# Optimization experiments

Hardware: AMD Instinct MI355X
Metric: run time of the kernel (lower is better)

## Reference

```python
import jax, jax.numpy as jnp
import numpy as np

EMBED_DIM = 256
NUM_EMB = 4096
LIMIT = 0.01


def setup_inputs() -> dict:
    key = jax.random.key(0)
    k1, k2 = jax.random.split(key)
    x = jax.random.normal(k1, (32, 32, 32, EMBED_DIM), dtype=jnp.float32)
    # codebook initialized uniform(-limit, limit), stored as [D, K] like the torch module
    vectors = jax.random.uniform(k2, (EMBED_DIM, NUM_EMB), dtype=jnp.float32,
                                 minval=-LIMIT, maxval=LIMIT)
    return {"x": x, "vectors": vectors}


def reference(x, vectors):
    B = x.shape[0]
    flat_x = x.reshape(-1, EMBED_DIM)                       # [N, D]
    distances = (jnp.sum(flat_x * flat_x, axis=1, keepdims=True)
                 - 2.0 * flat_x @ vectors
                 + jnp.sum(vectors * vectors, axis=0, keepdims=True))
    encoding_indices = jnp.argmin(distances, axis=1)        # [N]
    quantized_flat = vectors.T[encoding_indices]            # gather rows of [K, D]
    quantized_x = quantized_flat.reshape(x.shape)
    dictionary_loss = jnp.mean((jax.lax.stop_gradient(x) - quantized_x) ** 2)
    commitment_loss = jnp.mean((x - jax.lax.stop_gradient(quantized_x)) ** 2)
    # straight-through estimator
    quantized_x = x + jax.lax.stop_gradient(quantized_x - x)
    return (quantized_x, dictionary_loss, commitment_loss,
            encoding_indices.reshape(B, -1))
```

## Files before the change

kernel.cpp:

```cpp
#include <hip/hip_runtime.h>
#include <math.h>

#define D_DIM 256
#define K_NUM 4096
#define N_ROWS 32768
#define QCAP 3072
#define MARGIN 0.02f

typedef _Float16 half8 __attribute__((ext_vector_type(8)));
typedef float floatx4 __attribute__((ext_vector_type(4)));

__global__ __launch_bounds__(256) void vq_vv(const float* __restrict__ V,
                                             float* __restrict__ vv) {
  int k = blockIdx.x * 256 + threadIdx.x;
  float acc = 0.0f;
  for (int d = 0; d < D_DIM; ++d) {
    float v = V[(size_t)d * K_NUM + k];
    acc = __fadd_rn(acc, __fmul_rn(v, v));
  }
  vv[k] = acc;
}

__global__ __launch_bounds__(256) void vq_prep(const float* __restrict__ V,
                                               _Float16* __restrict__ vtb,
                                               float* __restrict__ vt,
                                               int write_vt) {
  __shared__ float tile[64][64];
  const int col0 = (blockIdx.x & 63) * 64;
  const int d0 = (blockIdx.x >> 6) * 64;
  const int cq = threadIdx.x >> 6;
  const int cl = threadIdx.x & 63;
#pragma unroll
  for (int it = 0; it < 16; ++it) {
    int d = it * 4 + cq;
    tile[d][cl] = V[(size_t)(d0 + d) * K_NUM + col0 + cl];
  }
  __syncthreads();
#pragma unroll
  for (int qq = 0; qq < 2; ++qq) {
    int q = cq * 2 + qq;
    half8 h;
#pragma unroll
    for (int j = 0; j < 8; ++j) h[j] = (_Float16)tile[q * 8 + j][cl];
    *(half8*)(vtb + ((size_t)(d0 / 8 + q) * K_NUM + col0 + cl) * 8) = h;
  }
  if (write_vt) {
#pragma unroll
    for (int j = 0; j < 4; ++j) {
      int d = cq * 16 + j * 4;
      float4 f;
      f.x = tile[d + 0][cl]; f.y = tile[d + 1][cl];
      f.z = tile[d + 2][cl]; f.w = tile[d + 3][cl];
      *(float4*)(vt + (size_t)(col0 + cl) * D_DIM + d0 + d) = f;
    }
  }
}

struct alignas(16) ScreenShared {
  _Float16 a[64 * 256];
  float vvs[K_NUM];
  float xxs[64];
  float wmin[8][64];
  float thr[64];
  unsigned long long best[64];
  unsigned qbuf[QCAP];
  int qn;
};

__device__ __forceinline__ void vq_push(ScreenShared& sh, int r, int col) {
  int u = atomicAdd(&sh.qn, 1);
  if (u < QCAP) sh.qbuf[u] = ((unsigned)r << 12) | (unsigned)col;
}

template <int MODE>
__device__ __forceinline__ void vq_cell(ScreenShared& sh,
                                        const _Float16* __restrict__ vtb,
                                        float* tb, int w, int l, int c) {
  const int g = l >> 4, ln = l & 15;
  const int cb = w * 512 + c * 32;
  const float vv0 = sh.vvs[cb + ln];
  const float vv1 = sh.vvs[cb + 16 + ln];

  const int abase = (ln << 8) ^ ((g ^ (ln & 7)) << 3);
  const char* bp = (const char*)vtb + (((size_t)g * K_NUM + cb + ln) << 4);

  floatx4 acc[4][2];
#pragma unroll
  for (int rf = 0; rf < 4; ++rf)
#pragma unroll
    for (int cf = 0; cf < 2; ++cf) acc[rf][cf] = {0.f, 0.f, 0.f, 0.f};

  half8 afb[2][4], bfb[2][2];
  bfb[0][0] = *(const half8*)bp;
  bfb[0][1] = *(const half8*)(bp + 256);
#pragma unroll
  for (int rf = 0; rf < 4; ++rf)
    afb[0][rf] = *(const half8*)(sh.a + abase + rf * 4096);

#pragma unroll
  for (int ks = 0; ks < 8; ++ks) {
    const int cur = ks & 1, nxt = cur ^ 1;
    if (ks < 7) {
      const int koff = (ks + 1) * 262144;
      bfb[nxt][0] = *(const half8*)(bp + koff);
      bfb[nxt][1] = *(const half8*)(bp + koff + 256);
      const int aoff = abase ^ ((ks + 1) << 5);
#pragma unroll
      for (int rf = 0; rf < 4; ++rf)
        afb[nxt][rf] = *(const half8*)(sh.a + aoff + rf * 4096);
    }
#pragma unroll
    for (int rf = 0; rf < 4; ++rf)
#pragma unroll
      for (int cf = 0; cf < 2; ++cf)
        acc[rf][cf] = __builtin_amdgcn_mfma_f32_16x16x32_f16(
            afb[cur][rf], bfb[cur][cf], acc[rf][cf], 0, 0, 0);
  }

#pragma unroll
  for (int rf = 0; rf < 4; ++rf) {
#pragma unroll
    for (int reg = 0; reg < 4; ++reg) {
      float s0v = fmaf(-2.0f, acc[rf][0][reg], vv0);
      float s1v = fmaf(-2.0f, acc[rf][1][reg], vv1);
      float m = fminf(s0v, s1v);
      if (MODE == 0) {
        tb[rf * 4 + reg] = fminf(tb[rf * 4 + reg], m);
      } else {
        float thr = tb[rf * 4 + reg];
        if (m <= thr) {
          const int r = rf * 16 + g * 4 + reg;
          if (s0v <= thr) vq_push(sh, r, cb + ln);
          if (s1v <= thr) vq_push(sh, r, cb + 16 + ln);
        }
      }
    }
  }
}

__global__ __launch_bounds__(512, 4) void vq_screen(
    const float* __restrict__ X, const float* __restrict__ V,
    const _Float16* __restrict__ vtb, const float* __restrict__ vvp,
    const float* __restrict__ vt, float* __restrict__ idx_out,
    float* __restrict__ outq, float* __restrict__ loss_sum) {
  __shared__ ScreenShared sh;
  const int tid = threadIdx.x;
  const int w = tid >> 6, l = tid & 63;
  const int row0 = blockIdx.x * 64;

#pragma unroll
  for (int it = 0; it < 4; ++it) {
    int idx = it * 512 + tid;
    int r = idx >> 5, s = idx & 31;
    const float* xp = X + (size_t)(row0 + r) * D_DIM + s * 8;
    float4 v0 = *(const float4*)xp, v1 = *(const float4*)(xp + 4);
    half8 h;
    h[0] = (_Float16)v0.x; h[1] = (_Float16)v0.y;
    h[2] = (_Float16)v0.z; h[3] = (_Float16)v0.w;
    h[4] = (_Float16)v1.x; h[5] = (_Float16)v1.y;
    h[6] = (_Float16)v1.z; h[7] = (_Float16)v1.w;
    int slot = (r << 5) | (s ^ (r & 7));
    *(half8*)&sh.a[slot * 8] = h;
  }
#pragma unroll
  for (int it = 0; it < 8; ++it) sh.vvs[it * 512 + tid] = vvp[it * 512 + tid];

  {
    const int grp = tid >> 4;
    const int half = (l >> 3) & 1, j = l & 7;
#pragma unroll
    for (int rr = 0; rr < 2; ++rr) {
      const int r = grp * 2 + rr;
      const float* p = X + (size_t)(row0 + r) * D_DIM + half * 128 + j;
      float v = p[0];
      float acc = __fmul_rn(v, v);
#pragma unroll
      for (int i = 1; i < 16; ++i) {
        v = p[i * 8];
        acc = __fadd_rn(acc, __fmul_rn(v, v));
      }
      acc = __fadd_rn(acc, __shfl_xor(acc, 1));
      acc = __fadd_rn(acc, __shfl_xor(acc, 2));
      acc = __fadd_rn(acc, __shfl_xor(acc, 4));
      acc = __fadd_rn(acc, __shfl_xor(acc, 8));
      if ((l & 15) == 0) sh.xxs[r] = acc;
    }
  }
  if (tid < 64) sh.best[tid] = 0xFFFFFFFFFFFFFFFFull;
  if (tid == 0) sh.qn = 0;
  __syncthreads();

  float tb[16];
#pragma unroll
  for (int i = 0; i < 16; ++i) tb[i] = INFINITY;

  vq_cell<0>(sh, vtb, tb, w, l, 0);
  vq_cell<0>(sh, vtb, tb, w, l, 8);

#pragma unroll
  for (int i = 0; i < 16; ++i) {
#pragma unroll
    for (int off = 1; off <= 8; off <<= 1)
      tb[i] = fminf(tb[i], __shfl_xor(tb[i], off));
  }
  {
    const int g = l >> 4, ln = l & 15;
    if (ln == 0) {
#pragma unroll
      for (int rf = 0; rf < 4; ++rf)
#pragma unroll
        for (int reg = 0; reg < 4; ++reg)
          sh.wmin[w][rf * 16 + g * 4 + reg] = tb[rf * 4 + reg];
    }
  }
  __syncthreads();
  if (tid < 64) {
    float m = sh.wmin[0][tid];
#pragma unroll
    for (int j = 1; j < 8; ++j) m = fminf(m, sh.wmin[j][tid]);
    sh.thr[tid] = m + MARGIN;
  }
  __syncthreads();
  {
    const int g = l >> 4;
#pragma unroll
    for (int rf = 0; rf < 4; ++rf)
#pragma unroll
      for (int reg = 0; reg < 4; ++reg)
        tb[rf * 4 + reg] = sh.thr[rf * 16 + g * 4 + reg];
  }

  for (int c = 0; c < 16; ++c) vq_cell<1>(sh, vtb, tb, w, l, c);
  __syncthreads();

  const int nq = min(sh.qn, QCAP);
  for (int i = w; i < nq; i += 8) {
    unsigned e = sh.qbuf[i];
    int r = (int)(e >> 12), col = (int)(e & 4095);
    float4 xv = *(const float4*)(X + (size_t)(row0 + r) * D_DIM + l * 4);
    float p = 0.f;
    if (vt) {
      float4 qv = *(const float4*)(vt + (size_t)col * D_DIM + l * 4);
      p = fmaf(xv.x, qv.x, p);
      p = fmaf(xv.y, qv.y, p);
      p = fmaf(xv.z, qv.z, p);
      p = fmaf(xv.w, qv.w, p);
    } else {
      const float* vp = V + col;
      p = fmaf(xv.x, vp[(size_t)(l * 4 + 0) * K_NUM], p);
      p = fmaf(xv.y, vp[(size_t)(l * 4 + 1) * K_NUM], p);
      p = fmaf(xv.z, vp[(size_t)(l * 4 + 2) * K_NUM], p);
      p = fmaf(xv.w, vp[(size_t)(l * 4 + 3) * K_NUM], p);
    }
#pragma unroll
    for (int off = 1; off < 64; off <<= 1) p += __shfl_xor(p, off);
    if (l == 0) {
      float s = __fadd_rn(__fsub_rn(sh.xxs[r], __fmul_rn(2.0f, p)),
                          sh.vvs[col]);
      unsigned long long key =
          ((unsigned long long)__float_as_uint(s) << 32) | (unsigned)col;
      atomicMin(&sh.best[r], key);
    }
  }
  __syncthreads();

  if (tid < 64)
    idx_out[row0 + tid] = (float)(unsigned)(sh.best[tid] & 0xFFFFFFFFu);

  float lsum = 0.f;
#pragma unroll
  for (int it = 0; it < 8; ++it) {
    int t = it * 512 + tid;
    int rloc = t >> 6;
    int c4 = (t & 63) << 2;
    int bi = (int)(unsigned)(sh.best[rloc] & 0xFFFFFFFFu);
    float4 xv = *(const float4*)(X + (size_t)(row0 + rloc) * D_DIM + c4);
    float4 qv;
    if (vt) {
      qv = *(const float4*)(vt + (size_t)bi * D_DIM + c4);
    } else {
      qv.x = V[(size_t)(c4 + 0) * K_NUM + bi];
      qv.y = V[(size_t)(c4 + 1) * K_NUM + bi];
      qv.z = V[(size_t)(c4 + 2) * K_NUM + bi];
      qv.w = V[(size_t)(c4 + 3) * K_NUM + bi];
    }
    float4 o;
    o.x = __fadd_rn(xv.x, __fsub_rn(qv.x, xv.x));
    o.y = __fadd_rn(xv.y, __fsub_rn(qv.y, xv.y));
    o.z = __fadd_rn(xv.z, __fsub_rn(qv.z, xv.z));
    o.w = __fadd_rn(xv.w, __fsub_rn(qv.w, xv.w));
    *(float4*)(outq + (size_t)(row0 + rloc) * D_DIM + c4) = o;
    float d0 = __fsub_rn(xv.x, qv.x), d1 = __fsub_rn(xv.y, qv.y);
    float d2 = __fsub_rn(xv.z, qv.z), d3 = __fsub_rn(xv.w, qv.w);
    lsum += d0 * d0 + d1 * d1 + d2 * d2 + d3 * d3;
  }
#pragma unroll
  for (int off = 1; off < 64; off <<= 1) lsum += __shfl_xor(lsum, off);
  __syncthreads();
  float* red = (float*)sh.qbuf;
  if (l == 0) red[w] = lsum;
  __syncthreads();
  if (tid == 0) {
    float s = red[0];
#pragma unroll
    for (int j = 1; j < 8; ++j) s += red[j];
    atomicAdd(loss_sum, s);
  }
}

__global__ void vq_fin(const float* __restrict__ loss_sum,
                       float* __restrict__ out_losses) {
  float m = loss_sum[0] / 8388608.0f;
  out_losses[0] = m;
  out_losses[1] = m;
}

extern "C" void kernel_launch(void* const* d_in, const int* in_sizes, int n_in,
                              void* d_out, int out_size, void* d_ws, size_t ws_size,
                              hipStream_t stream) {
  const float* x = (const float*)d_in[0];
  const float* V = (const float*)d_in[1];
  float* out = (float*)d_out;
  float* outq    = out;
  float* outloss = out + 8388608;
  float* outidx  = out + 8388610;

  float* ws_vv  = (float*)d_ws;
  float* ws_sum = ws_vv + K_NUM;
  _Float16* ws_vtb = (_Float16*)((char*)d_ws + 163840);
  float* ws_vt = (float*)((char*)d_ws + 163840 + 2097152);
  const int have_vt = (ws_size >= (size_t)(163840 + 2097152 + 4194304));
  float* vt_arg = have_vt ? ws_vt : (float*)nullptr;

  hipMemsetAsync(ws_sum, 0, sizeof(float), stream);
  vq_vv    <<<K_NUM / 256, 256, 0, stream>>>(V, ws_vv);
  vq_prep  <<<256, 256, 0, stream>>>(V, ws_vtb, ws_vt, have_vt);
  vq_screen<<<N_ROWS / 64, 512, 0, stream>>>(x, V, ws_vtb, ws_vv, vt_arg,
                                             outidx, outq, ws_sum);
  vq_fin   <<<1, 1, 0, stream>>>(ws_sum, outloss);
}
```

Measured before the change: 196.7 us.

## Triple-buffer codebook fragments, raise MFMA priority, use nontemporal epilogue memory ops

The B-fragment prefetch in the MFMA distance cell moves from double to triple buffering, so global codebook loads are issued two k-steps ahead. The MFMA block is wrapped in s_setprio to favour matrix issue over other waves. The rescoring and output epilogue now use nontemporal loads and stores for X, the transposed codebook, and the quantized output, to reduce cache pollution. Together these add register pressure and may lower occupancy. The nontemporal hint on the reused codebook rows could also hurt cache hits.

```diff
diff --git a/kernel.cpp b/kernel.cpp
--- a/kernel.cpp
+++ b/kernel.cpp
@@ -90,31 +90,36 @@
 #pragma unroll
     for (int cf = 0; cf < 2; ++cf) acc[rf][cf] = {0.f, 0.f, 0.f, 0.f};
 
-  half8 afb[2][4], bfb[2][2];
+  half8 afb[2][4], bfb[3][2];
   bfb[0][0] = *(const half8*)bp;
   bfb[0][1] = *(const half8*)(bp + 256);
+  bfb[1][0] = *(const half8*)(bp + 262144);
+  bfb[1][1] = *(const half8*)(bp + 262144 + 256);
 #pragma unroll
   for (int rf = 0; rf < 4; ++rf)
     afb[0][rf] = *(const half8*)(sh.a + abase + rf * 4096);
 
 #pragma unroll
   for (int ks = 0; ks < 8; ++ks) {
-    const int cur = ks & 1, nxt = cur ^ 1;
+    if (ks < 6) {
+      const int koff = (ks + 2) * 262144;
+      bfb[(ks + 2) % 3][0] = *(const half8*)(bp + koff);
+      bfb[(ks + 2) % 3][1] = *(const half8*)(bp + koff + 256);
+    }
     if (ks < 7) {
-      const int koff = (ks + 1) * 262144;
-      bfb[nxt][0] = *(const half8*)(bp + koff);
-      bfb[nxt][1] = *(const half8*)(bp + koff + 256);
       const int aoff = abase ^ ((ks + 1) << 5);
 #pragma unroll
       for (int rf = 0; rf < 4; ++rf)
-        afb[nxt][rf] = *(const half8*)(sh.a + aoff + rf * 4096);
-    }
+        afb[(ks + 1) & 1][rf] = *(const half8*)(sh.a + aoff + rf * 4096);
+    }
+    __builtin_amdgcn_s_setprio(1);
 #pragma unroll
     for (int rf = 0; rf < 4; ++rf)
 #pragma unroll
       for (int cf = 0; cf < 2; ++cf)
         acc[rf][cf] = __builtin_amdgcn_mfma_f32_16x16x32_f16(
-            afb[cur][rf], bfb[cur][cf], acc[rf][cf], 0, 0, 0);
+            afb[ks & 1][rf], bfb[ks % 3][cf], acc[rf][cf], 0, 0, 0);
+    __builtin_amdgcn_s_setprio(0);
   }
 
 #pragma unroll
@@ -167,11 +172,11 @@
 
   {
     const int grp = tid >> 4;
-    const int half = (l >> 3) & 1, j = l & 7;
+    const int hv = (l >> 3) & 1, j = l & 7;
 #pragma unroll
     for (int rr = 0; rr < 2; ++rr) {
       const int r = grp * 2 + rr;
-      const float* p = X + (size_t)(row0 + r) * D_DIM + half * 128 + j;
+      const float* p = X + (size_t)(row0 + r) * D_DIM + hv * 128 + j;
       float v = p[0];
       float acc = __fmul_rn(v, v);
 #pragma unroll
@@ -240,11 +245,12 @@
     float4 xv = *(const float4*)(X + (size_t)(row0 + r) * D_DIM + l * 4);
     float p = 0.f;
     if (vt) {
-      float4 qv = *(const float4*)(vt + (size_t)col * D_DIM + l * 4);
-      p = fmaf(xv.x, qv.x, p);
-      p = fmaf(xv.y, qv.y, p);
-      p = fmaf(xv.z, qv.z, p);
-      p = fmaf(xv.w, qv.w, p);
+      floatx4 qv = __builtin_nontemporal_load(
+          (const floatx4*)(vt + (size_t)col * D_DIM + l * 4));
+      p = fmaf(xv.x, qv[0], p);
+      p = fmaf(xv.y, qv[1], p);
+      p = fmaf(xv.z, qv[2], p);
+      p = fmaf(xv.w, qv[3], p);
     } else {
       const float* vp = V + col;
       p = fmaf(xv.x, vp[(size_t)(l * 4 + 0) * K_NUM], p);
@@ -274,22 +280,28 @@
     int rloc = t >> 6;
     int c4 = (t & 63) << 2;
     int bi = (int)(unsigned)(sh.best[rloc] & 0xFFFFFFFFu);
-    float4 xv = *(const float4*)(X + (size_t)(row0 + rloc) * D_DIM + c4);
+    floatx4 xv4 = __builtin_nontemporal_load(
+        (const floatx4*)(X + (size_t)(row0 + rloc) * D_DIM + c4));
+    float4 xv;
+    xv.x = xv4[0]; xv.y = xv4[1]; xv.z = xv4[2]; xv.w = xv4[3];
     float4 qv;
     if (vt) {
-      qv = *(const float4*)(vt + (size_t)bi * D_DIM + c4);
+      floatx4 qv4 = __builtin_nontemporal_load(
+          (const floatx4*)(vt + (size_t)bi * D_DIM + c4));
+      qv.x = qv4[0]; qv.y = qv4[1]; qv.z = qv4[2]; qv.w = qv4[3];
     } else {
       qv.x = V[(size_t)(c4 + 0) * K_NUM + bi];
       qv.y = V[(size_t)(c4 + 1) * K_NUM + bi];
       qv.z = V[(size_t)(c4 + 2) * K_NUM + bi];
       qv.w = V[(size_t)(c4 + 3) * K_NUM + bi];
     }
-    float4 o;
-    o.x = __fadd_rn(xv.x, __fsub_rn(qv.x, xv.x));
-    o.y = __fadd_rn(xv.y, __fsub_rn(qv.y, xv.y));
-    o.z = __fadd_rn(xv.z, __fsub_rn(qv.z, xv.z));
-    o.w = __fadd_rn(xv.w, __fsub_rn(qv.w, xv.w));
-    *(float4*)(outq + (size_t)(row0 + rloc) * D_DIM + c4) = o;
+    floatx4 o;
+    o[0] = __fadd_rn(xv.x, __fsub_rn(qv.x, xv.x));
+    o[1] = __fadd_rn(xv.y, __fsub_rn(qv.y, xv.y));
+    o[2] = __fadd_rn(xv.z, __fsub_rn(qv.z, xv.z));
+    o[3] = __fadd_rn(xv.w, __fsub_rn(qv.w, xv.w));
+    __builtin_nontemporal_store(
+        o, (floatx4*)(outq + (size_t)(row0 + rloc) * D_DIM + c4));
     float d0 = __fsub_rn(xv.x, qv.x), d1 = __fsub_rn(xv.y, qv.y);
     float d2 = __fsub_rn(xv.z, qv.z), d3 = __fsub_rn(xv.w, qv.w);
     lsum += d0 * d0 + d1 * d1 + d2 * d2 + d3 * d3;
```

Measured after the change: 217.0 us. 1.1x slower.
